# Optimization experiments

Hardware: AMD Instinct MI355X
Metric: run time of the kernel (lower is better)

The kernel has to match this reference:

```python
import jax, jax.numpy as jnp
import numpy as np

SENTINEL = 24635
NUM_ENTITIES = 24636
EMB_DIM = 128


def setup_inputs() -> dict:
    key = jax.random.key(0)
    ks = jax.random.split(key, 6)
    B, L = 4096, 50
    return {
        "encoded_context_embs": jax.random.normal(ks[0], (B, 1024), jnp.float32),
        "ent_embs": jax.random.normal(ks[1], (NUM_ENTITIES, EMB_DIM), jnp.float32) * 0.02,
        "W1": jax.random.normal(ks[2], (768, 1024), jnp.float32) * 0.02,
        "W2": jax.random.normal(ks[3], (512, 768), jnp.float32) * 0.02,
        "W3": jax.random.normal(ks[4], (128, 512), jnp.float32) * 0.02,
        "ent_list": jax.random.randint(ks[5], (B, L), 0, NUM_ENTITIES, jnp.int64),
    }


def reference(encoded_context_embs, ent_embs, W1, W2, W3, ent_list):
    # --- ragged gather + masked mean with sentinel early-exit ---
    # valid[b, l] == 1 iff no sentinel appeared at positions <= l (prefix-AND)
    not_sent = (ent_list != SENTINEL).astype(ent_embs.dtype)   # [B, L]
    valid = jnp.cumprod(not_sent, axis=1)                      # [B, L]
    gathered = ent_embs[ent_list]                              # [B, L, D]
    cnt = valid.sum(axis=1)                                    # [B]
    summed = jnp.einsum("bl,bld->bd", valid, gathered)        # [B, D]
    mean = summed / jnp.maximum(cnt, 1.0)[:, None]
    # sentinel at position 0 -> fall back to the sentinel embedding
    user_embs = jnp.where((cnt == 0)[:, None], ent_embs[SENTINEL][None, :], mean)

    # --- MLP on pooled context: 1024 -> 768 -> 512 -> 128 ---
    x = jax.nn.relu(encoded_context_embs @ W1.T)
    x = jax.nn.relu(x @ W2.T)
    q = x @ W3.T                                               # [B, 128]

    # --- cross attention: query=q, key=value=user_embs ---
    scale = 1.0 / jnp.sqrt(jnp.asarray(q.shape[-1], q.dtype))
    scores = (q @ user_embs.T) * scale                         # [B, B]
    weights = jax.nn.softmax(scores, axis=-1)
    return weights @ user_embs                                 # [B, 128]
```

## Files before the change

kernel.cpp:

```cpp
#include <hip/hip_runtime.h>
#include <hip/hip_bf16.h>

#define SENTINEL 24635

typedef unsigned char f8_t;
using bf16x8  = __attribute__((ext_vector_type(8))) __bf16;
using bf16x2  = __attribute__((ext_vector_type(2))) __bf16;
using floatx4 = __attribute__((ext_vector_type(4))) float;

__device__ inline int pack4_fp8(float4 a, float s) {
  int w = __builtin_amdgcn_cvt_pk_fp8_f32(a.x * s, a.y * s, 0, false);
  return __builtin_amdgcn_cvt_pk_fp8_f32(a.z * s, a.w * s, w, true);
}

__device__ inline void store_fp8x8(f8_t* d, float4 a, float4 b, float s) {
  int2 v; v.x = pack4_fp8(a, s); v.y = pack4_fp8(b, s);
  *(int2*)d = v;
}

__device__ inline void gll16(const void* g, void* l) {
  __builtin_amdgcn_global_load_lds(
      (const __attribute__((address_space(1))) unsigned int*)g,
      (__attribute__((address_space(3))) unsigned int*)l, 16, 0, 0);
}

__global__ __launch_bounds__(256) void prep_kernel(
    const float* __restrict__ s0, f8_t* __restrict__ d0,
    const float* __restrict__ s1, f8_t* __restrict__ d1,
    const float* __restrict__ ent, const int* __restrict__ ent_list,
    __bf16* __restrict__ user_n) {
  if (blockIdx.x < 2432) {
    int g = blockIdx.x * 256 + threadIdx.x;
    const float* s; f8_t* d; int i; float sc;
    if (g < 524288)      { s = s0; d = d0; i = g;          sc = 1.f;  }
    else                 { s = s1; d = d1; i = g - 524288; sc = 16.f; }
    i *= 8;
    float4 a = *(const float4*)(s + i);
    float4 b = *(const float4*)(s + i + 4);
    store_fp8x8(d + i, a, b, sc);
    return;
  }
  const int b = (blockIdx.x - 2432) * 4 + (threadIdx.x >> 6);
  const int lane = threadIdx.x & 63;
  int myidx = (lane < 50) ? ent_list[b * 50 + lane] : 0;
  unsigned long long m = __ballot(lane < 50 && myidx == SENTINEL);
  const int cnt = (m == 0) ? 50 : (int)__builtin_ctzll(m);

  float sx = 0.f, sy = 0.f;
  for (int l0 = 0; l0 < 50; l0 += 10) {
    if (l0 >= cnt) break;
    float2 e[10];
#pragma unroll
    for (int j = 0; j < 10; ++j) {
      int idx = __shfl(myidx, l0 + j);
      e[j] = *(const float2*)(ent + (size_t)idx * 128 + lane * 2);
    }
#pragma unroll
    for (int j = 0; j < 10; ++j) {
      if (l0 + j < cnt) { sx += e[j].x; sy += e[j].y; }
    }
  }
  float vx, vy;
  if (cnt == 0) {
    float2 e = *(const float2*)(ent + (size_t)SENTINEL * 128 + lane * 2);
    vx = e.x; vy = e.y;
  } else {
    float inv = 1.f / (float)cnt;
    vx = sx * inv; vy = sy * inv;
  }
  bf16x2 o; o[0] = (__bf16)vx; o[1] = (__bf16)vy;
  *(bf16x2*)(user_n + (size_t)b * 128 + lane * 2) = o;
}

template <int WR, int WC, int MT, int NT, int RELU, bool OUT_BF16, int NS>
__device__ inline void gemm_body_f8(const f8_t* __restrict__ A,
                                    const f8_t* __restrict__ W,
                                    void* __restrict__ Cout,
                                    int M, int N, int K, int bn0, int bm0,
                                    char* lds) {
  constexpr int BM = WR * MT * 16;
  constexpr int BN = WC * NT * 16;
  auto As = (f8_t (*)[BM][32])lds;
  auto Bs = (f8_t (*)[BN][32])(lds + (size_t)NS * BM * 32);
  const int tid  = threadIdx.x;
  const int w    = tid >> 6;
  const int lane = tid & 63;
  const int quad = lane >> 4;
  const int l16  = lane & 15;
  const int wr   = w / WC;
  const int wc   = w % WC;
  const int lrow = lane >> 1;
  const int lcol = (lane & 1) * 16;

  floatx4 acc[MT][NT];
#pragma unroll
  for (int mt = 0; mt < MT; ++mt)
#pragma unroll
    for (int nt = 0; nt < NT; ++nt) acc[mt][nt] = (floatx4){0.f, 0.f, 0.f, 0.f};

  constexpr int nAc = NS * (BM / 32);
  constexpr int nBc = NS * (BN / 32);
  for (int k0 = 0; k0 < K; k0 += NS * 32) {
    __syncthreads();
#pragma unroll
    for (int c = w; c < nAc; c += 4) {
      int s = c / (BM / 32);
      int r = (c % (BM / 32)) * 32;
      gll16(A + (size_t)(bm0 + r + lrow) * K + k0 + s * 32 + lcol, &As[s][r][0]);
    }
#pragma unroll
    for (int c = w; c < nBc; c += 4) {
      int s = c / (BN / 32);
      int r = (c % (BN / 32)) * 32;
      gll16(W + (size_t)(bn0 + r + lrow) * K + k0 + s * 32 + lcol, &Bs[s][r][0]);
    }
    __syncthreads();
#pragma unroll
    for (int s = 0; s < NS; ++s) {
      long af[MT], bfr[NT];
#pragma unroll
      for (int mt = 0; mt < MT; ++mt)
        af[mt] = *(const long*)&As[s][wr * (MT * 16) + mt * 16 + l16][quad * 8];
#pragma unroll
      for (int nt = 0; nt < NT; ++nt)
        bfr[nt] = *(const long*)&Bs[s][wc * (NT * 16) + nt * 16 + l16][quad * 8];
#pragma unroll
      for (int mt = 0; mt < MT; ++mt)
#pragma unroll
        for (int nt = 0; nt < NT; ++nt)
          acc[mt][nt] = __builtin_amdgcn_mfma_f32_16x16x32_fp8_fp8(
              af[mt], bfr[nt], acc[mt][nt], 0, 0, 0);
    }
  }

  const float osc = 0.0625f;
#pragma unroll
  for (int mt = 0; mt < MT; ++mt) {
    const int row0 = bm0 + wr * (MT * 16) + mt * 16 + quad * 4;
#pragma unroll
    for (int nt = 0; nt < NT; ++nt) {
      const int col = bn0 + wc * (NT * 16) + nt * 16 + l16;
#pragma unroll
      for (int r = 0; r < 4; ++r) {
        float v = acc[mt][nt][r] * osc;
        if (RELU) v = fmaxf(v, 0.f);
        if (OUT_BF16) {
          ((__bf16*)Cout)[(size_t)(row0 + r) * N + col] = (__bf16)v;
        } else {
          int p = __builtin_amdgcn_cvt_pk_fp8_f32(v, v, 0, false);
          ((f8_t*)Cout)[(size_t)(row0 + r) * N + col] = (f8_t)(p & 0xff);
        }
      }
    }
  }
}

template <int WR, int WC, int MT, int NT, int RELU, bool OUT_BF16, int NS>
__global__ __launch_bounds__(256) void gemm_f8(const f8_t* __restrict__ A,
                                               const f8_t* __restrict__ W,
                                               void* __restrict__ C,
                                               int M, int N, int K) {
  __shared__ char lds[(size_t)NS * ((WR * MT * 16) + (WC * NT * 16)) * 32];
  gemm_body_f8<WR, WC, MT, NT, RELU, OUT_BF16, NS>(
      A, W, C, M, N, K, blockIdx.x * (WC * NT * 16), blockIdx.y * (WR * MT * 16),
      lds);
}

__global__ __launch_bounds__(256) void gemm1_tr(const f8_t* __restrict__ A,
                                                const f8_t* __restrict__ W,
                                                f8_t* __restrict__ C,
                                                const __bf16* __restrict__ un,
                                                __bf16* __restrict__ ut,
                                                const float* __restrict__ s2,
                                                f8_t* __restrict__ d2,
                                                const float* __restrict__ s3,
                                                f8_t* __restrict__ d3) {
  __shared__ char lds[20480];
  const int bx = blockIdx.x;
  if (bx < 512) {
    gemm_body_f8<2, 2, 2, 3, 1, false, 4>(A, W, C, 4096, 768, 1024,
                                          (bx % 8) * 96, (bx / 8) * 64, lds);
    return;
  }
  if (bx >= 640) {
    int g = (bx - 640) * 256 + threadIdx.x;
    const float* s; f8_t* d; int i;
    if (g < 49152) { s = s2; d = d2; i = g; }
    else           { s = s3; d = d3; i = g - 49152; }
    i *= 8;
    float4 a = *(const float4*)(s + i);
    float4 b = *(const float4*)(s + i + 4);
    store_fp8x8(d + i, a, b, 16.f);
    return;
  }
  const int idx = bx - 512;
  const int r0 = (idx & 63) * 64;
  const int c0 = (idx >> 6) * 64;
  auto T = (__bf16 (*)[72])lds;
  const int tid = threadIdx.x;
#pragma unroll
  for (int p = 0; p < 2; ++p) {
    int r = (tid >> 3) + p * 32;
    int c = (tid & 7) * 8;
    *(bf16x8*)&T[r][c] = *(const bf16x8*)(un + (size_t)(r0 + r) * 128 + c0 + c);
  }
  __syncthreads();
#pragma unroll
  for (int p = 0; p < 2; ++p) {
    int c = (tid >> 3) + p * 32;
    int r = (tid & 7) * 8;
    bf16x8 v;
#pragma unroll
    for (int j = 0; j < 8; ++j) v[j] = T[r + j][c];
    *(bf16x8*)(ut + (size_t)(c0 + c) * 4096 + r0 + r) = v;
  }
}

__global__ __launch_bounds__(256) void flash_attn(const __bf16* __restrict__ Q,
                                                  const __bf16* __restrict__ Un_g,
                                                  const __bf16* __restrict__ Ut_g,
                                                  __bf16* __restrict__ O_part,
                                                  float* __restrict__ lp) {
  __shared__ __bf16 Un[64][136];
  __shared__ __bf16 Ut[128][72];
  __shared__ __bf16 Ps[4][32][72];
  const int tid  = threadIdx.x;
  const int w    = tid >> 6;
  const int lane = tid & 63;
  const int quad = lane >> 4;
  const int l16  = lane & 15;
  const int qrow0 = blockIdx.x * 128;
  const int split = blockIdx.y;
  const float scale = 0.08838834764831845f;

  bf16x8 aq[2][4];
#pragma unroll
  for (int mt = 0; mt < 2; ++mt)
#pragma unroll
    for (int c = 0; c < 4; ++c)
      aq[mt][c] = *(const bf16x8*)(Q + (size_t)(qrow0 + w * 32 + mt * 16 + l16) * 128 +
                                   c * 32 + quad * 8);

  floatx4 o[2][8];
#pragma unroll
  for (int mt = 0; mt < 2; ++mt)
#pragma unroll
    for (int t = 0; t < 8; ++t) o[mt][t] = (floatx4){0.f, 0.f, 0.f, 0.f};
  float lsum[2][4] = {{0.f, 0.f, 0.f, 0.f}, {0.f, 0.f, 0.f, 0.f}};

  const int sr = tid >> 4, sc = (tid & 15) * 8;
  const int td = tid >> 3, tk = (tid & 7) * 8;
  bf16x8 un_r[4], ut_r[4];

#define LD_CHUNK(key0)                                                         \
  do {                                                                         \
    _Pragma("unroll")                                                          \
    for (int p = 0; p < 4; ++p)                                                \
      un_r[p] = *(const bf16x8*)(Un_g + (size_t)((key0) + sr + p * 16) * 128 + sc); \
    _Pragma("unroll")                                                          \
    for (int p = 0; p < 4; ++p)                                                \
      ut_r[p] = *(const bf16x8*)(Ut_g + (size_t)(td + p * 32) * 4096 + (key0) + tk); \
  } while (0)

#define ST_CHUNK()                                                             \
  do {                                                                         \
    _Pragma("unroll")                                                          \
    for (int p = 0; p < 4; ++p) *(bf16x8*)&Un[sr + p * 16][sc] = un_r[p];      \
    _Pragma("unroll")                                                          \
    for (int p = 0; p < 4; ++p) *(bf16x8*)&Ut[td + p * 32][tk] = ut_r[p];      \
  } while (0)

  LD_CHUNK(split * 256);
  ST_CHUNK();
  __syncthreads();

  for (int chunk = 0; chunk < 4; ++chunk) {
    if (chunk < 3) LD_CHUNK(split * 256 + (chunk + 1) * 64);

#pragma unroll
    for (int t = 0; t < 4; ++t) {
      bf16x8 bk[4];
#pragma unroll
      for (int c = 0; c < 4; ++c)
        bk[c] = *(const bf16x8*)&Un[t * 16 + l16][c * 32 + quad * 8];
      floatx4 s0 = (floatx4){0.f, 0.f, 0.f, 0.f};
      floatx4 s1 = (floatx4){0.f, 0.f, 0.f, 0.f};
      __builtin_amdgcn_s_setprio(1);
#pragma unroll
      for (int c = 0; c < 4; ++c) {
        s0 = __builtin_amdgcn_mfma_f32_16x16x32_bf16(aq[0][c], bk[c], s0, 0, 0, 0);
        s1 = __builtin_amdgcn_mfma_f32_16x16x32_bf16(aq[1][c], bk[c], s1, 0, 0, 0);
      }
      __builtin_amdgcn_s_setprio(0);
#pragma unroll
      for (int r = 0; r < 4; ++r) {
        float p0 = __expf(s0[r] * scale);
        float p1 = __expf(s1[r] * scale);
        lsum[0][r] += p0;
        lsum[1][r] += p1;
        Ps[w][quad * 4 + r][t * 16 + l16] = (__bf16)p0;
        Ps[w][16 + quad * 4 + r][t * 16 + l16] = (__bf16)p1;
      }
    }

#pragma unroll
    for (int c2 = 0; c2 < 2; ++c2) {
      bf16x8 ap0 = *(const bf16x8*)&Ps[w][l16][c2 * 32 + quad * 8];
      bf16x8 ap1 = *(const bf16x8*)&Ps[w][16 + l16][c2 * 32 + quad * 8];
      __builtin_amdgcn_s_setprio(1);
#pragma unroll
      for (int dt = 0; dt < 8; ++dt) {
        bf16x8 bv = *(const bf16x8*)&Ut[dt * 16 + l16][c2 * 32 + quad * 8];
        o[0][dt] = __builtin_amdgcn_mfma_f32_16x16x32_bf16(ap0, bv, o[0][dt], 0, 0, 0);
        o[1][dt] = __builtin_amdgcn_mfma_f32_16x16x32_bf16(ap1, bv, o[1][dt], 0, 0, 0);
      }
      __builtin_amdgcn_s_setprio(0);
    }

    if (chunk < 3) {
      __syncthreads();
      ST_CHUNK();
      __syncthreads();
    }
  }
#undef LD_CHUNK
#undef ST_CHUNK

#pragma unroll
  for (int mt = 0; mt < 2; ++mt)
#pragma unroll
    for (int r = 0; r < 4; ++r) {
      float v = lsum[mt][r];
      v += __shfl_xor(v, 1);
      v += __shfl_xor(v, 2);
      v += __shfl_xor(v, 4);
      v += __shfl_xor(v, 8);
      lsum[mt][r] = v;
    }

  __bf16* Ob = O_part + (size_t)split * 524288;
#pragma unroll
  for (int mt = 0; mt < 2; ++mt) {
    const int row0 = qrow0 + w * 32 + mt * 16 + quad * 4;
#pragma unroll
    for (int dt = 0; dt < 8; ++dt) {
#pragma unroll
      for (int r = 0; r < 4; ++r) {
        Ob[(size_t)(row0 + r) * 128 + dt * 16 + l16] = (__bf16)o[mt][dt][r];
      }
    }
    if (l16 == 0) {
#pragma unroll
      for (int r = 0; r < 4; ++r) lp[(size_t)split * 4096 + row0 + r] = lsum[mt][r];
    }
  }
}

__global__ __launch_bounds__(256) void combine_kernel(const __bf16* __restrict__ Op,
                                                      const float* __restrict__ lp,
                                                      float* __restrict__ out) {
  const int i = (blockIdx.x * 256 + threadIdx.x) * 8;
  const int row = i >> 7;
  float num[8] = {0.f, 0.f, 0.f, 0.f, 0.f, 0.f, 0.f, 0.f};
  float den = 0.f;
#pragma unroll
  for (int s = 0; s < 16; ++s) {
    bf16x8 v = *(const bf16x8*)(Op + (size_t)s * 524288 + i);
#pragma unroll
    for (int j = 0; j < 8; ++j) num[j] += (float)v[j];
    den += lp[(size_t)s * 4096 + row];
  }
  float inv = 1.f / den;
  float4 r0 = {num[0] * inv, num[1] * inv, num[2] * inv, num[3] * inv};
  float4 r1 = {num[4] * inv, num[5] * inv, num[6] * inv, num[7] * inv};
  *(float4*)(out + i) = r0;
  *(float4*)(out + i + 4) = r1;
}

extern "C" void kernel_launch(void* const* d_in, const int* in_sizes, int n_in,
                              void* d_out, int out_size, void* d_ws, size_t ws_size,
                              hipStream_t stream) {
  (void)in_sizes; (void)n_in; (void)out_size; (void)ws_size;
  const float* ctx      = (const float*)d_in[0];
  const float* ent_embs = (const float*)d_in[1];
  const float* W1       = (const float*)d_in[2];
  const float* W2       = (const float*)d_in[3];
  const float* W3       = (const float*)d_in[4];
  const int*   ent_list = (const int*)d_in[5];
  float* out = (float*)d_out;

  char* base = (char*)d_ws;
  __bf16* user_n = (__bf16*)(base);
  __bf16* user_t = (__bf16*)(base + (1ull << 20));
  __bf16* qb     = (__bf16*)(base + (2ull << 20));
  float*  lp     = (float*)(base + (3ull << 20));
  f8_t*   ctxb   = (f8_t*)(base + (4ull << 20));
  f8_t*   W1b    = (f8_t*)(base + (8ull << 20));
  f8_t*   W2b    = (f8_t*)(base + 9175040ull);
  f8_t*   W3b    = (f8_t*)(base + 9568256ull);
  f8_t*   x1b    = (f8_t*)(base + (10ull << 20));
  f8_t*   x2b    = (f8_t*)(base + (13ull << 20));
  __bf16* O_part = (__bf16*)(base + (15ull << 20));

  prep_kernel<<<3456, 256, 0, stream>>>(ctx, ctxb, W1, W1b,
                                        ent_embs, ent_list, user_n);
  gemm1_tr<<<864, 256, 0, stream>>>(ctxb, W1b, x1b, user_n, user_t,
                                    W2, W2b, W3, W3b);
  gemm_f8<2, 2, 2, 2, 1, false, 4><<<dim3(8, 64), 256, 0, stream>>>(
      x1b, W2b, x2b, 4096, 512, 768);
  gemm_f8<2, 2, 1, 1, 0, true, 4><<<dim3(4, 128), 256, 0, stream>>>(
      x2b, W3b, qb, 4096, 128, 512);
  flash_attn<<<dim3(32, 16), 256, 0, stream>>>(qb, user_n, user_t, O_part, lp);
  combine_kernel<<<256, 256, 0, stream>>>(O_part, lp, out);
}
```

Before: 148.4 us.

## Rebalance independent work across kernels: pool with GEMM1, transpose with GEMM2

Moves the entity gather/mean pooling out of the fp8 conversion prep kernel and into the GEMM1 launch as extra blocks. The user-embedding transpose moves from the GEMM1 launch into a new combined GEMM2 launch. The aim is to overlap the memory-bound pooling and transpose with compute-bound GEMM blocks and to shorten the serial critical path. The kernel count stays the same. Heterogeneous blocks in one launch may cause tail imbalance.

New measurement: 141.1 us. -5.0%, faster.

```diff
diff --git a/kernel.cpp b/kernel.cpp
--- a/kernel.cpp
+++ b/kernel.cpp
@@ -24,23 +24,9 @@
       (__attribute__((address_space(3))) unsigned int*)l, 16, 0, 0);
 }
 
-__global__ __launch_bounds__(256) void prep_kernel(
-    const float* __restrict__ s0, f8_t* __restrict__ d0,
-    const float* __restrict__ s1, f8_t* __restrict__ d1,
-    const float* __restrict__ ent, const int* __restrict__ ent_list,
-    __bf16* __restrict__ user_n) {
-  if (blockIdx.x < 2432) {
-    int g = blockIdx.x * 256 + threadIdx.x;
-    const float* s; f8_t* d; int i; float sc;
-    if (g < 524288)      { s = s0; d = d0; i = g;          sc = 1.f;  }
-    else                 { s = s1; d = d1; i = g - 524288; sc = 16.f; }
-    i *= 8;
-    float4 a = *(const float4*)(s + i);
-    float4 b = *(const float4*)(s + i + 4);
-    store_fp8x8(d + i, a, b, sc);
-    return;
-  }
-  const int b = (blockIdx.x - 2432) * 4 + (threadIdx.x >> 6);
+__device__ inline void pool_body(const float* __restrict__ ent,
+                                 const int* __restrict__ ent_list,
+                                 __bf16* __restrict__ user_n, int b) {
   const int lane = threadIdx.x & 63;
   int myidx = (lane < 50) ? ent_list[b * 50 + lane] : 0;
   unsigned long long m = __ballot(lane < 50 && myidx == SENTINEL);
@@ -70,6 +56,19 @@
   }
   bf16x2 o; o[0] = (__bf16)vx; o[1] = (__bf16)vy;
   *(bf16x2*)(user_n + (size_t)b * 128 + lane * 2) = o;
+}
+
+__global__ __launch_bounds__(256) void prep_kernel(
+    const float* __restrict__ s0, f8_t* __restrict__ d0,
+    const float* __restrict__ s1, f8_t* __restrict__ d1) {
+  int g = blockIdx.x * 256 + threadIdx.x;
+  const float* s; f8_t* d; int i; float sc;
+  if (g < 524288)      { s = s0; d = d0; i = g;          sc = 1.f;  }
+  else                 { s = s1; d = d1; i = g - 524288; sc = 16.f; }
+  i *= 8;
+  float4 a = *(const float4*)(s + i);
+  float4 b = *(const float4*)(s + i + 4);
+  store_fp8x8(d + i, a, b, sc);
 }
 
 template <int WR, int WC, int MT, int NT, int RELU, bool OUT_BF16, int NS>
@@ -166,15 +165,16 @@
       lds);
 }
 
-__global__ __launch_bounds__(256) void gemm1_tr(const f8_t* __restrict__ A,
-                                                const f8_t* __restrict__ W,
-                                                f8_t* __restrict__ C,
-                                                const __bf16* __restrict__ un,
-                                                __bf16* __restrict__ ut,
-                                                const float* __restrict__ s2,
-                                                f8_t* __restrict__ d2,
-                                                const float* __restrict__ s3,
-                                                f8_t* __restrict__ d3) {
+__global__ __launch_bounds__(256) void gemm1_pool(const f8_t* __restrict__ A,
+                                                  const f8_t* __restrict__ W,
+                                                  f8_t* __restrict__ C,
+                                                  const float* __restrict__ ent,
+                                                  const int* __restrict__ ent_list,
+                                                  __bf16* __restrict__ user_n,
+                                                  const float* __restrict__ s2,
+                                                  f8_t* __restrict__ d2,
+                                                  const float* __restrict__ s3,
+                                                  f8_t* __restrict__ d3) {
   __shared__ char lds[20480];
   const int bx = blockIdx.x;
   if (bx < 512) {
@@ -182,15 +182,30 @@
                                           (bx % 8) * 96, (bx / 8) * 64, lds);
     return;
   }
-  if (bx >= 640) {
-    int g = (bx - 640) * 256 + threadIdx.x;
-    const float* s; f8_t* d; int i;
-    if (g < 49152) { s = s2; d = d2; i = g; }
-    else           { s = s3; d = d3; i = g - 49152; }
-    i *= 8;
-    float4 a = *(const float4*)(s + i);
-    float4 b = *(const float4*)(s + i + 4);
-    store_fp8x8(d + i, a, b, 16.f);
+  if (bx < 1536) {
+    pool_body(ent, ent_list, user_n, (bx - 512) * 4 + (threadIdx.x >> 6));
+    return;
+  }
+  int g = (bx - 1536) * 256 + threadIdx.x;
+  const float* s; f8_t* d; int i;
+  if (g < 49152) { s = s2; d = d2; i = g; }
+  else           { s = s3; d = d3; i = g - 49152; }
+  i *= 8;
+  float4 a = *(const float4*)(s + i);
+  float4 b = *(const float4*)(s + i + 4);
+  store_fp8x8(d + i, a, b, 16.f);
+}
+
+__global__ __launch_bounds__(256) void gemm2_tr(const f8_t* __restrict__ A,
+                                                const f8_t* __restrict__ W,
+                                                f8_t* __restrict__ C,
+                                                const __bf16* __restrict__ un,
+                                                __bf16* __restrict__ ut) {
+  __shared__ char lds[16384];
+  const int bx = blockIdx.x;
+  if (bx < 512) {
+    gemm_body_f8<2, 2, 2, 2, 1, false, 4>(A, W, C, 4096, 512, 768,
+                                          (bx % 8) * 64, (bx / 8) * 64, lds);
     return;
   }
   const int idx = bx - 512;
@@ -402,12 +417,10 @@
   f8_t*   x2b    = (f8_t*)(base + (13ull << 20));
   __bf16* O_part = (__bf16*)(base + (15ull << 20));
 
-  prep_kernel<<<3456, 256, 0, stream>>>(ctx, ctxb, W1, W1b,
-                                        ent_embs, ent_list, user_n);
-  gemm1_tr<<<864, 256, 0, stream>>>(ctxb, W1b, x1b, user_n, user_t,
-                                    W2, W2b, W3, W3b);
-  gemm_f8<2, 2, 2, 2, 1, false, 4><<<dim3(8, 64), 256, 0, stream>>>(
-      x1b, W2b, x2b, 4096, 512, 768);
+  prep_kernel<<<2432, 256, 0, stream>>>(ctx, ctxb, W1, W1b);
+  gemm1_pool<<<1760, 256, 0, stream>>>(ctxb, W1b, x1b, ent_embs, ent_list,
+                                       user_n, W2, W2b, W3, W3b);
+  gemm2_tr<<<640, 256, 0, stream>>>(x1b, W2b, x2b, user_n, user_t);
   gemm_f8<2, 2, 1, 1, 0, true, 4><<<dim3(4, 128), 256, 0, stream>>>(
       x2b, W3b, qb, 4096, 128, 512);
   flash_attn<<<dim3(32, 16), 256, 0, stream>>>(qb, user_n, user_t, O_part, lp);
```
